# Performance work log

Hardware: AMD Instinct MI355X
Metric: run time of the kernel (lower is better)

Reference implementation:

```python
import jax, jax.numpy as jnp
import numpy as np
import string

N_QUBITS = 16
N_LAYERS = 2
BATCH = 32
DIM = 2 ** N_QUBITS


def _apply_1q(psi, U, q):
    # psi: (B,) + (2,)*n complex; U: (2,2) complex acting on qubit q
    n = psi.ndim - 1
    ax = string.ascii_lowercase[:n]
    out = list(ax)
    out[q] = 'A'
    return jnp.einsum('A' + ax[q] + ',z' + ax + '->z' + ''.join(out), U, psi)


def _apply_2q(psi, G, c, t):
    # G: (2,2,2,2) = (out_c, out_t, in_c, in_t)
    n = psi.ndim - 1
    ax = string.ascii_lowercase[:n]
    out = list(ax)
    out[c] = 'A'
    out[t] = 'B'
    return jnp.einsum('AB' + ax[c] + ax[t] + ',z' + ax + '->z' + ''.join(out), G, psi)


def _rx(th):
    c = jnp.cos(th * 0.5).astype(jnp.complex64)
    s = jnp.sin(th * 0.5).astype(jnp.complex64)
    return jnp.array([[c, -1j * s], [-1j * s, c]])


def _ry(th):
    c = jnp.cos(th * 0.5).astype(jnp.complex64)
    s = jnp.sin(th * 0.5).astype(jnp.complex64)
    return jnp.array([[c, -s], [s, c]])


def _rz(th):
    th_c = th.astype(jnp.complex64)
    z = jnp.zeros((), jnp.complex64)
    return jnp.array([[jnp.exp(-0.5j * th_c), z], [z, jnp.exp(0.5j * th_c)]])


_CNOT = jnp.array([[1, 0, 0, 0],
                   [0, 1, 0, 0],
                   [0, 0, 0, 1],
                   [0, 0, 1, 0]], dtype=jnp.complex64).reshape(2, 2, 2, 2)


def setup_inputs() -> dict:
    key = jax.random.key(0)
    k1, k2, k3 = jax.random.split(key, 3)
    thetas = jax.random.normal(k1, (N_LAYERS, 3, N_QUBITS), dtype=jnp.float32)
    re = jax.random.normal(k2, (BATCH, DIM), dtype=jnp.float32)
    im = jax.random.normal(k3, (BATCH, DIM), dtype=jnp.float32)
    norm = jnp.sqrt(jnp.sum(re * re + im * im, axis=-1, keepdims=True))
    return {"thetas": thetas, "state_re": re / norm, "state_im": im / norm}


def reference(thetas, state_re, state_im):
    B = state_re.shape[0]
    psi = (state_re.astype(jnp.complex64) + 1j * state_im.astype(jnp.complex64))
    psi = psi.reshape((B,) + (2,) * N_QUBITS)
    for l in range(N_LAYERS):
        for q in range(N_QUBITS):
            psi = _apply_1q(psi, _rx(thetas[l, 0, q]), q)
            psi = _apply_1q(psi, _ry(thetas[l, 1, q]), q)
            psi = _apply_1q(psi, _rz(thetas[l, 2, q]), q)
        for q in range(N_QUBITS):
            psi = _apply_2q(psi, _CNOT, q, (q + 1) % N_QUBITS)
    probs = (psi.real ** 2 + psi.imag ** 2).reshape(B, -1)
    return probs
```

## Files before the change

### kernel.cpp

```cpp
#include <hip/hip_runtime.h>


#define NT 256

__device__ __forceinline__ int fperm(int x) {
  int y = x ^ (x >> 1);
  y ^= (x & 1) ? 0xC000 : 0;
  return y & 0xFFFF;
}

__device__ __forceinline__ int finv16(int x) {
  int s = x;
  s ^= s >> 1; s ^= s >> 2; s ^= s >> 4; s ^= s >> 8;
  int b15 = ((s ^ (s >> 15)) & 1) << 15;
  return (s & 0x7FFF) | b15;
}

__device__ __forceinline__ int swz1(int l) { return l ^ ((l >> 4) & 31); }
__device__ __forceinline__ int swz2(int l) { return l ^ ((l >> 5) & 31); }

__device__ __forceinline__ void compute_gates(const float* __restrict__ th, float* gsh) {
  int tid = threadIdx.x;
  if (tid < 32) {
    int l = tid >> 4, q = tid & 15;
    float tx = th[l * 48 + q], ty = th[l * 48 + 16 + q], tz = th[l * 48 + 32 + q];
    float cx, sx, cy, sy, cz, sz;
    sincosf(0.5f * tx, &sx, &cx);
    sincosf(0.5f * ty, &sy, &cy);
    sincosf(0.5f * tz, &sz, &cz);
    float m00r = cy * cx, m00i =  sy * sx;
    float m01r = -sy * cx, m01i = -cy * sx;
    float m10r =  sy * cx, m10i = -cy * sx;
    float m11r =  cy * cx, m11i = -sy * sx;
    float* G = gsh + tid * 8;
    G[0] = cz * m00r + sz * m00i;  G[1] = cz * m00i - sz * m00r;
    G[2] = cz * m01r + sz * m01i;  G[3] = cz * m01i - sz * m01r;
    G[4] = cz * m10r - sz * m10i;  G[5] = cz * m10i + sz * m10r;
    G[6] = cz * m11r - sz * m11i;  G[7] = cz * m11i + sz * m11r;
  }
}

template <int MK, int SK, int N>
__device__ __forceinline__ void greg(float (&ar)[N], float (&ai)[N],
                                     const float* G, int c) {
  const float4* G4 = (const float4*)G;
  float4 r0 = G4[0], r1 = G4[1];
  bool sw = (c != 0);
  float h00r = sw ? r1.z : r0.x, h00i = sw ? r1.w : r0.y;
  float h01r = sw ? r1.x : r0.z, h01i = sw ? r1.y : r0.w;
  float h10r = sw ? r0.z : r1.x, h10i = sw ? r0.w : r1.y;
  float h11r = sw ? r0.x : r1.z, h11i = sw ? r0.y : r1.w;
  constexpr int PV = MK & (-MK);
#pragma unroll
  for (int k = 0; k < N; k++) {
    if (k & PV) continue;
    const int k2 = k ^ MK;
    const int p0 = __builtin_popcount(k & SK) & 1;
    const int ka = p0 ? k2 : k;
    const int kb = p0 ? k : k2;
    float xr = ar[ka], xi = ai[ka], yr = ar[kb], yi = ai[kb];
    ar[ka] = h00r * xr - h00i * xi + h01r * yr - h01i * yi;
    ai[ka] = h00r * xi + h00i * xr + h01r * yi + h01i * yr;
    ar[kb] = h10r * xr - h10i * xi + h11r * yr - h11i * yi;
    ai[kb] = h10r * xi + h10i * xr + h11r * yi + h11i * yr;
  }
}


__device__ __forceinline__ void phaseA_body(int t, int bbase, int wb,
                                            const float* gsh,
                                            float* sre, float* sim,
                                            const float* __restrict__ xre,
                                            const float* __restrict__ xim,
                                            float2* __restrict__ ws) {
  float ar[16], ai[16];
  int base = bbase + (wb << 12);
  const float4* xr4 = (const float4*)(xre + base + (t << 4));
  const float4* xi4 = (const float4*)(xim + base + (t << 4));
#pragma unroll
  for (int q = 0; q < 4; q++) {
    float4 v = xr4[q]; ar[4*q] = v.x; ar[4*q+1] = v.y; ar[4*q+2] = v.z; ar[4*q+3] = v.w;
    float4 w = xi4[q]; ai[4*q] = w.x; ai[4*q+1] = w.y; ai[4*q+2] = w.z; ai[4*q+3] = w.w;
  }
  __syncthreads();
  greg<1, 1>(ar, ai, gsh + 15 * 8, 0);
  greg<2, 2>(ar, ai, gsh + 14 * 8, 0);
  greg<4, 4>(ar, ai, gsh + 13 * 8, 0);
  greg<8, 8>(ar, ai, gsh + 12 * 8, 0);
#pragma unroll
  for (int k = 0; k < 16; k++) { int s = swz1((t << 4) | k); sre[s] = ar[k]; sim[s] = ai[k]; }
  __syncthreads();
#pragma unroll
  for (int k = 0; k < 16; k++) {
    int s = swz1((t & 15) | (k << 4) | ((t >> 4) << 8));
    ar[k] = sre[s]; ai[k] = sim[s];
  }
  greg<1, 1>(ar, ai, gsh + 11 * 8, 0);
  greg<2, 2>(ar, ai, gsh + 10 * 8, 0);
  greg<4, 4>(ar, ai, gsh + 9 * 8, 0);
  greg<8, 8>(ar, ai, gsh + 8 * 8, 0);
#pragma unroll
  for (int k = 0; k < 16; k++) {
    int s = swz1((t & 15) | (k << 4) | ((t >> 4) << 8));
    sre[s] = ar[k]; sim[s] = ai[k];
  }
  __syncthreads();
#pragma unroll
  for (int k = 0; k < 16; k++) {
    int s = swz1(t | (k << 8)); ar[k] = sre[s]; ai[k] = sim[s];
  }
  greg<1, 1>(ar, ai, gsh + 7 * 8, 0);
  greg<2, 2>(ar, ai, gsh + 6 * 8, 0);
  greg<4, 4>(ar, ai, gsh + 5 * 8, 0);
  greg<8, 8>(ar, ai, gsh + 4 * 8, 0);
#pragma unroll
  for (int k = 0; k < 16; k++)
    ws[base + t + (k << 8)] = make_float2(ar[k], ai[k]);
}

__device__ __forceinline__ void phaseB_body(int t, int bbase, int wb,
                                            const float* gsh,
                                            float* sre, float* sim,
                                            float2* __restrict__ ws) {
  float ar[16], ai[16];
#pragma unroll
  for (int k = 0; k < 16; k++) {
    float2 v = ws[bbase + t + (wb << 8) + (k << 12)];
    ar[k] = v.x; ai[k] = v.y;
  }
  int cA = (__popc(t) + __popc(wb)) & 1;
  greg<1, 1>(ar, ai, gsh + 3 * 8, 0);
  greg<2, 2>(ar, ai, gsh + 2 * 8, 0);
  greg<4, 4>(ar, ai, gsh + 1 * 8, 0);
  greg<8, 8>(ar, ai, gsh + 0 * 8, 0);
  greg<12, 7>(ar, ai, gsh + (16 + 0) * 8, cA);
  greg<6, 12>(ar, ai, gsh + (16 + 1) * 8, 0);
  greg<3, 14>(ar, ai, gsh + (16 + 2) * 8, 0);
  __syncthreads();
#pragma unroll
  for (int k = 0; k < 16; k++) {
    int s = swz2(t | (k << 8)); sre[s] = ar[k]; sim[s] = ai[k];
  }
  __syncthreads();
#pragma unroll
  for (int k = 0; k < 16; k++) {
    int s = swz2((k & 3) | (t << 2) | ((k >> 2) << 10));
    ar[k] = sre[s]; ai[k] = sim[s];
  }
  greg<13, 15>(ar, ai, gsh + (16 + 15) * 8, cA);
  greg<3, 14>(ar, ai, gsh + (16 + 14) * 8, cA);
#pragma unroll
  for (int k = 0; k < 16; k++) {
    int s = swz2((k & 3) | (t << 2) | ((k >> 2) << 10));
    sre[s] = ar[k]; sim[s] = ai[k];
  }
  __syncthreads();
#pragma unroll
  for (int k = 0; k < 16; k++) {
    int s = swz2((t & 1) | (k << 1) | ((t >> 1) << 5));
    ar[k] = sre[s]; ai[k] = sim[s];
  }
  {
    int cC = (__popc(t >> 1) + __popc(wb)) & 1;
    greg<3, 14>(ar, ai, gsh + (16 + 13) * 8, cC);
    greg<6, 12>(ar, ai, gsh + (16 + 12) * 8, cC);
    greg<12, 8>(ar, ai, gsh + (16 + 11) * 8, cC);
  }
#pragma unroll
  for (int k = 0; k < 16; k++) {
    int s = swz2((t & 1) | (k << 1) | ((t >> 1) << 5));
    sre[s] = ar[k]; sim[s] = ai[k];
  }
  __syncthreads();
#pragma unroll
  for (int k = 0; k < 16; k++) {
    int s = swz2((t & 15) | (k << 4) | ((t >> 4) << 8));
    ar[k] = sre[s]; ai[k] = sim[s];
  }
  {
    int cD = (__popc(t >> 4) + __popc(wb)) & 1;
    greg<3, 14>(ar, ai, gsh + (16 + 10) * 8, cD);
    greg<6, 12>(ar, ai, gsh + (16 + 9) * 8, cD);
    greg<12, 8>(ar, ai, gsh + (16 + 8) * 8, cD);
  }
#pragma unroll
  for (int k = 0; k < 16; k++) {
    int full = (t & 15) | (k << 4) | (wb << 8) | ((t >> 4) << 12);
    ws[bbase + full] = make_float2(ar[k], ai[k]);
  }
}

__device__ __forceinline__ void phaseC_body(int t, int bbase3, int g3,
                                            const float* gsh,
                                            const float2* __restrict__ ws,
                                            float* __restrict__ out) {
  int jt = t | (g3 << 13);
  float br[32], bi[32];
#pragma unroll
  for (int k = 0; k < 32; k++) {
    int j = jt | (k << 8);
    float2 v = ws[bbase3 + fperm(j)];
    br[k] = v.x; bi[k] = v.y;
  }
  greg<1, 1>(br, bi, gsh + (16 + 7) * 8, 0);
  greg<2, 2>(br, bi, gsh + (16 + 6) * 8, 0);
  greg<4, 4>(br, bi, gsh + (16 + 5) * 8, 0);
  greg<8, 8>(br, bi, gsh + (16 + 4) * 8, 0);
  greg<16, 16>(br, bi, gsh + (16 + 3) * 8, 0);
#pragma unroll
  for (int k = 0; k < 32; k++) {
    int j = jt | (k << 8);
    out[bbase3 + finv16(j)] = br[k] * br[k] + bi[k] * bi[k];
  }
}


__global__ void __launch_bounds__(NT) pass1_k(const float* __restrict__ th,
                                              const float* __restrict__ xre,
                                              const float* __restrict__ xim,
                                              float2* __restrict__ ws) {
  __shared__ float gsh[256];
  __shared__ float sre[4096], sim[4096];
  int t = threadIdx.x;
  int blk = blockIdx.x, batch = blk >> 4, wb = blk & 15;
  compute_gates(th, gsh);
  phaseA_body(t, batch * 65536, wb, gsh, sre, sim, xre, xim, ws);
}

__global__ void __launch_bounds__(NT) pass2_k(const float* __restrict__ th,
                                              float2* __restrict__ ws) {
  __shared__ float gsh[256];
  __shared__ float sre[4096], sim[4096];
  int t = threadIdx.x;
  int blk = blockIdx.x, batch = blk >> 4, wb = blk & 15;
  compute_gates(th, gsh);
  __syncthreads();
  phaseB_body(t, batch * 65536, wb, gsh, sre, sim, ws);
}

__global__ void __launch_bounds__(NT) pass3_k(const float* __restrict__ th,
                                              const float2* __restrict__ ws,
                                              float* __restrict__ out) {
  __shared__ float gsh[256];
  int t = threadIdx.x;
  int blk = blockIdx.x, batch = blk >> 3, g3 = blk & 7;
  compute_gates(th, gsh);
  __syncthreads();
  phaseC_body(t, batch * 65536, g3, gsh, ws, out);
}


extern "C" void kernel_launch(void* const* d_in, const int* in_sizes, int n_in,
                              void* d_out, int out_size, void* d_ws, size_t ws_size,
                              hipStream_t stream) {
  const float* th  = (const float*)d_in[0];
  const float* xre = (const float*)d_in[1];
  const float* xim = (const float*)d_in[2];
  float* out = (float*)d_out;

  float2* amp = (float2*)d_ws;

  pass1_k<<<512, NT, 0, stream>>>(th, xre, xim, amp);
  pass2_k<<<512, NT, 0, stream>>>(th, amp);
  pass3_k<<<256, NT, 0, stream>>>(th, amp, out);
}
```

Baseline: 103.8 us.

## Use 512-thread pass1 with wavefront shuffles replacing one LDS transpose

Pass 1 now runs 512 threads per block with 8 amplitudes per thread instead of 16, on the same 4096-amplitude tile. Six of the twelve qubit gates are applied through cross-lane __shfl_xor exchanges, so only one shared-memory transpose and one block barrier are needed instead of two of each. This targets LDS traffic and synchronisation in the first pass, in exchange for extra shuffle instructions and more threads per block. It relies on the lane-to-qubit mapping of the shuffles matching the gate indices, which is non-trivial to verify.

Measured after the change: 105.7 us. About the same (+1.9%).

```diff
diff --git a/kernel.cpp b/kernel.cpp
--- a/kernel.cpp
+++ b/kernel.cpp
@@ -66,57 +66,24 @@
   }
 }
 
-
-__device__ __forceinline__ void phaseA_body(int t, int bbase, int wb,
-                                            const float* gsh,
-                                            float* sre, float* sim,
-                                            const float* __restrict__ xre,
-                                            const float* __restrict__ xim,
-                                            float2* __restrict__ ws) {
-  float ar[16], ai[16];
-  int base = bbase + (wb << 12);
-  const float4* xr4 = (const float4*)(xre + base + (t << 4));
-  const float4* xi4 = (const float4*)(xim + base + (t << 4));
-#pragma unroll
-  for (int q = 0; q < 4; q++) {
-    float4 v = xr4[q]; ar[4*q] = v.x; ar[4*q+1] = v.y; ar[4*q+2] = v.z; ar[4*q+3] = v.w;
-    float4 w = xi4[q]; ai[4*q] = w.x; ai[4*q+1] = w.y; ai[4*q+2] = w.z; ai[4*q+3] = w.w;
-  }
-  __syncthreads();
-  greg<1, 1>(ar, ai, gsh + 15 * 8, 0);
-  greg<2, 2>(ar, ai, gsh + 14 * 8, 0);
-  greg<4, 4>(ar, ai, gsh + 13 * 8, 0);
-  greg<8, 8>(ar, ai, gsh + 12 * 8, 0);
-#pragma unroll
-  for (int k = 0; k < 16; k++) { int s = swz1((t << 4) | k); sre[s] = ar[k]; sim[s] = ai[k]; }
-  __syncthreads();
-#pragma unroll
-  for (int k = 0; k < 16; k++) {
-    int s = swz1((t & 15) | (k << 4) | ((t >> 4) << 8));
-    ar[k] = sre[s]; ai[k] = sim[s];
-  }
-  greg<1, 1>(ar, ai, gsh + 11 * 8, 0);
-  greg<2, 2>(ar, ai, gsh + 10 * 8, 0);
-  greg<4, 4>(ar, ai, gsh + 9 * 8, 0);
-  greg<8, 8>(ar, ai, gsh + 8 * 8, 0);
-#pragma unroll
-  for (int k = 0; k < 16; k++) {
-    int s = swz1((t & 15) | (k << 4) | ((t >> 4) << 8));
-    sre[s] = ar[k]; sim[s] = ai[k];
-  }
-  __syncthreads();
-#pragma unroll
-  for (int k = 0; k < 16; k++) {
-    int s = swz1(t | (k << 8)); ar[k] = sre[s]; ai[k] = sim[s];
-  }
-  greg<1, 1>(ar, ai, gsh + 7 * 8, 0);
-  greg<2, 2>(ar, ai, gsh + 6 * 8, 0);
-  greg<4, 4>(ar, ai, gsh + 5 * 8, 0);
-  greg<8, 8>(ar, ai, gsh + 4 * 8, 0);
-#pragma unroll
-  for (int k = 0; k < 16; k++)
-    ws[base + t + (k << 8)] = make_float2(ar[k], ai[k]);
-}
+template <int M, int N>
+__device__ __forceinline__ void gshfl(float (&ar)[N], float (&ai)[N],
+                                      const float* G) {
+  const float4* G4 = (const float4*)G;
+  float4 r0 = G4[0], r1 = G4[1];
+  bool hi = (threadIdx.x & M) != 0;
+  float hsr = hi ? r1.z : r0.x, hsi = hi ? r1.w : r0.y;
+  float hpr = hi ? r1.x : r0.z, hpi = hi ? r1.y : r0.w;
+#pragma unroll
+  for (int k = 0; k < N; k++) {
+    float pr = __shfl_xor(ar[k], M, 64);
+    float pi = __shfl_xor(ai[k], M, 64);
+    float vr = ar[k], vi = ai[k];
+    ar[k] = hsr * vr - hsi * vi + hpr * pr - hpi * pi;
+    ai[k] = hsr * vi + hsi * vr + hpr * pi + hpi * pr;
+  }
+}
+
 
 __device__ __forceinline__ void phaseB_body(int t, int bbase, int wb,
                                             const float* gsh,
@@ -215,17 +182,63 @@
 }
 
 
-__global__ void __launch_bounds__(NT) pass1_k(const float* __restrict__ th,
-                                              const float* __restrict__ xre,
-                                              const float* __restrict__ xim,
-                                              float2* __restrict__ ws) {
+__global__ void __launch_bounds__(512) pass1_k(const float* __restrict__ th,
+                                               const float* __restrict__ xre,
+                                               const float* __restrict__ xim,
+                                               float2* __restrict__ ws) {
   __shared__ float gsh[256];
   __shared__ float sre[4096], sim[4096];
   int t = threadIdx.x;
   int blk = blockIdx.x, batch = blk >> 4, wb = blk & 15;
+  int base = batch * 65536 + (wb << 12);
+
   compute_gates(th, gsh);
-  phaseA_body(t, batch * 65536, wb, gsh, sre, sim, xre, xim, ws);
-}
+
+  float ar[8], ai[8];
+  const float4* xr4 = (const float4*)(xre + base + (t << 3));
+  const float4* xi4 = (const float4*)(xim + base + (t << 3));
+  {
+    float4 v0 = xr4[0], v1 = xr4[1];
+    float4 w0 = xi4[0], w1 = xi4[1];
+    ar[0] = v0.x; ar[1] = v0.y; ar[2] = v0.z; ar[3] = v0.w;
+    ar[4] = v1.x; ar[5] = v1.y; ar[6] = v1.z; ar[7] = v1.w;
+    ai[0] = w0.x; ai[1] = w0.y; ai[2] = w0.z; ai[3] = w0.w;
+    ai[4] = w1.x; ai[5] = w1.y; ai[6] = w1.z; ai[7] = w1.w;
+  }
+  __syncthreads();
+
+  greg<1, 1>(ar, ai, gsh + 15 * 8, 0);
+  greg<2, 2>(ar, ai, gsh + 14 * 8, 0);
+  greg<4, 4>(ar, ai, gsh + 13 * 8, 0);
+
+  gshfl<1> (ar, ai, gsh + 12 * 8);
+  gshfl<2> (ar, ai, gsh + 11 * 8);
+  gshfl<4> (ar, ai, gsh + 10 * 8);
+  gshfl<8> (ar, ai, gsh + 9 * 8);
+  gshfl<16>(ar, ai, gsh + 8 * 8);
+  gshfl<32>(ar, ai, gsh + 7 * 8);
+
+#pragma unroll
+  for (int k = 0; k < 8; k++) {
+    int s = swz1((t << 3) | k);
+    sre[s] = ar[k]; sim[s] = ai[k];
+  }
+  __syncthreads();
+#pragma unroll
+  for (int k = 0; k < 8; k++) {
+    int s = swz1(t | (k << 9));
+    ar[k] = sre[s]; ai[k] = sim[s];
+  }
+
+  greg<1, 1>(ar, ai, gsh + 6 * 8, 0);
+  greg<2, 2>(ar, ai, gsh + 5 * 8, 0);
+  greg<4, 4>(ar, ai, gsh + 4 * 8, 0);
+
+#pragma unroll
+  for (int k = 0; k < 8; k++)
+    ws[base + (t | (k << 9))] = make_float2(ar[k], ai[k]);
+}
+
 
 __global__ void __launch_bounds__(NT) pass2_k(const float* __restrict__ th,
                                               float2* __restrict__ ws) {
@@ -260,7 +273,7 @@
 
   float2* amp = (float2*)d_ws;
 
-  pass1_k<<<512, NT, 0, stream>>>(th, xre, xim, amp);
+  pass1_k<<<512, 512, 0, stream>>>(th, xre, xim, amp);
   pass2_k<<<512, NT, 0, stream>>>(th, amp);
   pass3_k<<<256, NT, 0, stream>>>(th, amp, out);
 }
```
